# Kernel tuning notes

Hardware: AMD Instinct MI355X
Metric: run time of the kernel (lower is better)

Reference implementation:

```python
import jax, jax.numpy as jnp
import numpy as np

B, T, D, H = 32, 2048, 256, 256  # batch, length, input_size, hidden_size


def _lstm_layer(x, W_ih, W_hh, b, reverse):
    """Single-direction LSTM over time. x: [B,T,Din]; W_ih: [4H,Din]; W_hh: [4H,H]; b: [4H].
    Gate order: i, f, g, o (PyTorch convention). Returns hidden states [B,T,H]."""
    # Precompute input contribution for all timesteps in one big GEMM.
    xg = jnp.einsum('btd,gd->btg', x, W_ih) + b  # [B,T,4H]
    Hh = W_hh.shape[1]
    Bb = x.shape[0]

    def step(carry, xg_t):
        h, c = carry
        g = xg_t + h @ W_hh.T  # [B,4H]
        i, f, gc, o = jnp.split(g, 4, axis=-1)
        c = jax.nn.sigmoid(f) * c + jax.nn.sigmoid(i) * jnp.tanh(gc)
        h = jax.nn.sigmoid(o) * jnp.tanh(c)
        return (h, c), h

    init = (jnp.zeros((Bb, Hh), x.dtype), jnp.zeros((Bb, Hh), x.dtype))
    _, hs = jax.lax.scan(step, init, jnp.swapaxes(xg, 0, 1), reverse=reverse)  # [T,B,H]
    return jnp.swapaxes(hs, 0, 1)  # [B,T,H]


def setup_inputs() -> dict:
    key = jax.random.key(0)
    ks = jax.random.split(key, 13)
    s = 0.05
    G = 4 * H
    inp = {
        'x': jax.random.normal(ks[0], (B, T, D), dtype=jnp.float32),
        # layer 0 (input size D), forward and reverse directions
        'W_ih_f0': jax.random.normal(ks[1], (G, D), dtype=jnp.float32) * s,
        'W_hh_f0': jax.random.normal(ks[2], (G, H), dtype=jnp.float32) * s,
        'b_f0': jnp.zeros((G,), dtype=jnp.float32),
        'W_ih_r0': jax.random.normal(ks[3], (G, D), dtype=jnp.float32) * s,
        'W_hh_r0': jax.random.normal(ks[4], (G, H), dtype=jnp.float32) * s,
        'b_r0': jnp.zeros((G,), dtype=jnp.float32),
        # layer 1 (input size 2H because bidirectional)
        'W_ih_f1': jax.random.normal(ks[5], (G, 2 * H), dtype=jnp.float32) * s,
        'W_hh_f1': jax.random.normal(ks[6], (G, H), dtype=jnp.float32) * s,
        'b_f1': jnp.zeros((G,), dtype=jnp.float32),
        'W_ih_r1': jax.random.normal(ks[7], (G, 2 * H), dtype=jnp.float32) * s,
        'W_hh_r1': jax.random.normal(ks[8], (G, H), dtype=jnp.float32) * s,
        'b_r1': jnp.zeros((G,), dtype=jnp.float32),
    }
    return inp


def reference(x, W_ih_f0, W_hh_f0, b_f0, W_ih_r0, W_hh_r0, b_r0,
              W_ih_f1, W_hh_f1, b_f1, W_ih_r1, W_hh_r1, b_r1):
    # Layer 0: bidirectional over raw input
    h0 = jnp.concatenate([
        _lstm_layer(x, W_ih_f0, W_hh_f0, b_f0, reverse=False),
        _lstm_layer(x, W_ih_r0, W_hh_r0, b_r0, reverse=True),
    ], axis=-1)  # [B,T,2H]
    # Layer 1: bidirectional over concatenated hidden states
    h1 = jnp.concatenate([
        _lstm_layer(h0, W_ih_f1, W_hh_f1, b_f1, reverse=False),
        _lstm_layer(h0, W_ih_r1, W_hh_r1, b_r1, reverse=True),
    ], axis=-1)  # [B,T,2H]
    return h1
```

## Files before the change

### kernel.cpp

```cpp
#include <hip/hip_runtime.h>
#include <stdint.h>


#define Bn 32
#define Tn 2048
#define Hn 256

typedef short short8 __attribute__((ext_vector_type(8)));
typedef float f32x4 __attribute__((ext_vector_type(4)));
typedef unsigned int u32x4 __attribute__((ext_vector_type(4)));

__device__ inline unsigned short f2b(float f) {
  union { float f; unsigned u; } v; v.f = f;
  unsigned r = v.u + 0x7fffu + ((v.u >> 16) & 1u);
  return (unsigned short)(r >> 16);
}
__device__ inline float asf(unsigned u) {
  union { unsigned u; float f; } v; v.u = u; return v.f;
}
__device__ inline float sigx(float x) {
  return __builtin_amdgcn_rcpf(1.f + __expf(-x));
}
__device__ inline float tanhx(float x) {
  return 2.f * __builtin_amdgcn_rcpf(1.f + __expf(-2.f * x)) - 1.f;
}

template <int K, bool AF32>
__global__ __launch_bounds__(256, 2) void xg_gemm(
    const void* __restrict__ Ain,
    const float* __restrict__ Wf, const float* __restrict__ bf_,
    const float* __restrict__ Wr, const float* __restrict__ br_,
    unsigned short* __restrict__ xg) {
  constexpr int KI = K / 32;
  const int bid = blockIdx.x;
  const int scan = bid & 1;
  const int sgrp = (bid >> 1) & 7;
  const int mchunk = bid >> 4;
  const int wave = threadIdx.x >> 6;
  const int lane = threadIdx.x & 63;
  const int l15 = lane & 15, quad = lane >> 4;
  const int stripe = sgrp * 4 + wave;
  const int gi0 = stripe * 32;
  const int wp = stripe & 7;
  const int gg = stripe >> 3;

  const float* W = scan ? Wr : Wf;
  const float* bias = scan ? br_ : bf_;

  short8 bfr[KI][2];
  float bias2[2];
#pragma unroll
  for (int sub = 0; sub < 2; ++sub) {
    const int gi = gi0 + sub * 16 + l15;
    bias2[sub] = bias[gi];
#pragma unroll
    for (int ki = 0; ki < KI; ++ki) {
      const float* src = W + (size_t)gi * K + ki * 32 + quad * 8;
      short8 v;
#pragma unroll
      for (int j = 0; j < 8; ++j) v[j] = (short)f2b(src[j]);
      bfr[ki][sub] = v;
    }
  }

  const size_t scanoff = (size_t)scan << 26;
#pragma unroll 1
  for (int mt0 = 0; mt0 < 16; ++mt0) {
    const int mt = mchunk * 16 + mt0;
    const size_t row = (size_t)mt * 16 + l15;
    f32x4 acc[2];
#pragma unroll
    for (int sub = 0; sub < 2; ++sub) {
      f32x4 bi = {bias2[sub], bias2[sub], bias2[sub], bias2[sub]};
      acc[sub] = bi;
    }
#pragma unroll
    for (int ki = 0; ki < KI; ++ki) {
      short8 af;
      if constexpr (AF32) {
        const float* ap = (const float*)Ain + row * K + ki * 32 + quad * 8;
        f32x4 a0 = *(const f32x4*)ap;
        f32x4 a1 = *(const f32x4*)(ap + 4);
#pragma unroll
        for (int j = 0; j < 4; ++j) { af[j] = (short)f2b(a0[j]); af[4 + j] = (short)f2b(a1[j]); }
      } else {
        const unsigned short* ap = (const unsigned short*)Ain + row * K + ki * 32 + quad * 8;
        af = *(const short8*)ap;
      }
#pragma unroll
      for (int sub = 0; sub < 2; ++sub)
        acc[sub] = __builtin_amdgcn_mfma_f32_16x16x32_bf16(af, bfr[ki][sub], acc[sub], 0, 0, 0);
    }
#pragma unroll
    for (int sub = 0; sub < 2; ++sub) {
#pragma unroll
      for (int r = 0; r < 4; ++r) {
        const int orow = mt * 16 + quad * 4 + r;
        const int m = orow >> 11, t = orow & 2047;
        size_t idx = scanoff
          + ((((size_t)t * 2 + (m >> 4)) * 8 + wp) << 11)
          + ((size_t)((((m >> 2) & 3) << 4) + l15) << 5)
          + (sub << 4) + (gg << 2) + (m & 3);
        xg[idx] = f2b(acc[sub][r]);
      }
    }
  }
}

template <bool LAYER1>
__global__ __launch_bounds__(512, 2) void lstm_scan(
    const unsigned short* __restrict__ xg,
    const float* __restrict__ Whh_f, const float* __restrict__ Whh_r,
    unsigned short* __restrict__ h0out,
    float* __restrict__ dout) {
  __shared__ __align__(16) char smem[131072 + 2 * 8448];

  const int bid = blockIdx.x;
  const int scan = bid & 1;
  const int mh = bid >> 1;
  const int wave = threadIdx.x >> 6;
  const int lane = threadIdx.x & 63;
  const int l15 = lane & 15, quad = lane >> 4;

  const float* Whh = scan ? Whh_r : Whh_f;

  short8 wres[2][3][8];
#pragma unroll
  for (int uh = 0; uh < 2; ++uh)
#pragma unroll
    for (int g = 0; g < 3; ++g)
#pragma unroll
      for (int ki = 0; ki < 8; ++ki) {
        const int col = g * 256 + wave * 32 + uh * 16 + l15;
        const float* src = Whh + ((size_t)col << 8) + ki * 32 + quad * 8;
        f32x4 a0 = *(const f32x4*)src;
        f32x4 a1 = *(const f32x4*)(src + 4);
        short8 v;
#pragma unroll
        for (int j = 0; j < 4; ++j) { v[j] = (short)f2b(a0[j]); v[4 + j] = (short)f2b(a1[j]); }
        wres[uh][g][ki] = v;
      }
#pragma unroll
  for (int uh = 0; uh < 2; ++uh)
#pragma unroll
    for (int ki = 0; ki < 8; ++ki) {
      const int col = 768 + wave * 32 + uh * 16 + l15;
      const float* src = Whh + ((size_t)col << 8) + ki * 32 + quad * 8;
      f32x4 a0 = *(const f32x4*)src;
      f32x4 a1 = *(const f32x4*)(src + 4);
      short8 v;
#pragma unroll
      for (int j = 0; j < 4; ++j) { v[j] = (short)f2b(a0[j]); v[4 + j] = (short)f2b(a1[j]); }
      *(short8*)(smem + ((((wave << 1) + uh) << 3) + ki) * 1024 + lane * 16) = v;
    }

  const size_t scanoff = (size_t)scan << 26;
  const int tstep = scan ? -1 : 1;
  const int t0 = scan ? (Tn - 1) : 0;
  const size_t lane_off = (size_t)lane * 32;
  u32x4 xr[2][2];
  {
    const unsigned short* xb =
        xg + scanoff + ((((size_t)t0 * 2 + mh) * 8 + wave) << 11) + lane_off;
    xr[0][0] = *(const u32x4*)(xb + 0);
    xr[0][1] = *(const u32x4*)(xb + 8);
    xr[1][0] = *(const u32x4*)(xb + 16);
    xr[1][1] = *(const u32x4*)(xb + 24);
  }

  char* hbuf = smem + 131072;
  float c_st[2][4] = {{0.f, 0.f, 0.f, 0.f}, {0.f, 0.f, 0.f, 0.f}};

  __syncthreads();

#pragma unroll 1
  for (int s = 0; s < Tn; ++s) {
    const int t = scan ? (Tn - 1 - s) : s;
    const int tn = (s < Tn - 1) ? (t + tstep) : t;
    const unsigned short* xbn =
        xg + scanoff + ((((size_t)tn * 2 + mh) * 8 + wave) << 11) + lane_off;
    const int p_r = (s - 1) & 1, p_w = s & 1;

#pragma unroll
    for (int uh = 0; uh < 2; ++uh) {
      f32x4 acc[4];
#pragma unroll
      for (int g = 0; g < 4; ++g) {
        unsigned lo = xr[uh][g >> 1][2 * (g & 1)];
        unsigned hi = xr[uh][g >> 1][2 * (g & 1) + 1];
        acc[g][0] = asf(lo << 16); acc[g][1] = asf(lo & 0xffff0000u);
        acc[g][2] = asf(hi << 16); acc[g][3] = asf(hi & 0xffff0000u);
      }
      if (uh == 1) {
        xr[0][0] = *(const u32x4*)(xbn + 0);
        xr[0][1] = *(const u32x4*)(xbn + 8);
      }

      if (s > 0) {
        const char* hr = hbuf + p_r * 8448 + l15 * 528 + quad * 16;
        const char* wl0 = smem + (((wave << 1) + uh) << 13) + lane * 16;
#pragma unroll
        for (int ki = 0; ki < 8; ++ki) {
          short8 a = *(const short8*)(hr + (ki << 6));
          short8 wl = *(const short8*)(wl0 + (ki << 10));
          acc[0] = __builtin_amdgcn_mfma_f32_16x16x32_bf16(a, wres[uh][0][ki], acc[0], 0, 0, 0);
          acc[1] = __builtin_amdgcn_mfma_f32_16x16x32_bf16(a, wres[uh][1][ki], acc[1], 0, 0, 0);
          acc[2] = __builtin_amdgcn_mfma_f32_16x16x32_bf16(a, wres[uh][2][ki], acc[2], 0, 0, 0);
          acc[3] = __builtin_amdgcn_mfma_f32_16x16x32_bf16(a, wl,              acc[3], 0, 0, 0);
        }
      }

      const int ubase = wave * 32 + uh * 16 + l15;
#pragma unroll
      for (int r = 0; r < 4; ++r) {
        float ig = sigx(acc[0][r]), fg = sigx(acc[1][r]);
        float gc = tanhx(acc[2][r]), og = sigx(acc[3][r]);
        float cv = fg * c_st[uh][r] + ig * gc;
        c_st[uh][r] = cv;
        float hv = og * tanhx(cv);
        unsigned short h16 = f2b(hv);
        int pk = __shfl_xor((int)h16, 1);
        const int row = quad * 4 + r;
        if (!(lane & 1)) {
          unsigned pv = (unsigned)h16 | ((unsigned)pk << 16);
          *(unsigned*)(hbuf + p_w * 8448 + row * 528 + ubase * 2) = pv;
        }
        const int b = mh * 16 + row;
        if constexpr (!LAYER1) {
          h0out[(((size_t)b * Tn + t) << 9) + scan * Hn + ubase] = h16;
        } else {
          dout[(((size_t)b * Tn + t) << 9) + scan * Hn + ubase] = hv;
        }
      }

      if (uh == 1) {
        xr[1][0] = *(const u32x4*)(xbn + 16);
        xr[1][1] = *(const u32x4*)(xbn + 24);
      }
    }

    __syncthreads();
  }
}

extern "C" void kernel_launch(void* const* d_in, const int* in_sizes, int n_in,
                              void* d_out, int out_size, void* d_ws, size_t ws_size,
                              hipStream_t stream) {
  (void)in_sizes; (void)n_in; (void)out_size; (void)ws_size;
  const float* x      = (const float*)d_in[0];
  const float* Wih_f0 = (const float*)d_in[1];
  const float* Whh_f0 = (const float*)d_in[2];
  const float* b_f0   = (const float*)d_in[3];
  const float* Wih_r0 = (const float*)d_in[4];
  const float* Whh_r0 = (const float*)d_in[5];
  const float* b_r0   = (const float*)d_in[6];
  const float* Wih_f1 = (const float*)d_in[7];
  const float* Whh_f1 = (const float*)d_in[8];
  const float* b_f1   = (const float*)d_in[9];
  const float* Wih_r1 = (const float*)d_in[10];
  const float* Whh_r1 = (const float*)d_in[11];
  const float* b_r1   = (const float*)d_in[12];

  char* ws = (char*)d_ws;
  unsigned short* xgbuf = (unsigned short*)ws;
  size_t off = (size_t)2 * Tn * Bn * 1024 * sizeof(unsigned short);
  unsigned short* h0out = (unsigned short*)(ws + off);

  dim3 blkA(256), blkB(512);
  xg_gemm<256, true><<<dim3(4096), blkA, 0, stream>>>(
      (const void*)x, Wih_f0, b_f0, Wih_r0, b_r0, xgbuf);
  lstm_scan<false><<<dim3(4), blkB, 0, stream>>>(
      xgbuf, Whh_f0, Whh_r0, h0out, (float*)nullptr);
  xg_gemm<512, false><<<dim3(4096), blkA, 0, stream>>>(
      (const void*)h0out, Wih_f1, b_f1, Wih_r1, b_r1, xgbuf);
  lstm_scan<true><<<dim3(4), blkB, 0, stream>>>(
      xgbuf, Whh_f1, Whh_r1, (unsigned short*)nullptr, (float*)d_out);
}
```

Before: 14.15 ms.

## Fold log2(e) scaling into weights and swizzle h buffer into MFMA fragment layout

Pre-scales the input and recurrent weights and biases by log2(e) (2·log2(e) for the cell gate) so the gate nonlinearities can call native exp2 directly, saving a multiply per transcendental on the serial per-step path. The cell state is kept scaled by 2·log2(e), which shifts the tanh into a sigmoid-based form. The hidden-state shared buffer moves from a padded row-major layout to a fragment-ordered layout, so each lane reads its MFMA A operand with one contiguous 16-byte load. The pre-scaling is applied before bf16 rounding, which slightly changes the numerics.

```diff
diff --git a/kernel.cpp b/kernel.cpp
--- a/kernel.cpp
+++ b/kernel.cpp
@@ -6,9 +6,15 @@
 #define Tn 2048
 #define Hn 256
 
+#define L2E 1.4426950408889634f
+#define L2E2 2.8853900817779268f
+#define L2E4 5.7707801635558535f
+
 typedef short short8 __attribute__((ext_vector_type(8)));
 typedef float f32x4 __attribute__((ext_vector_type(4)));
 typedef unsigned int u32x4 __attribute__((ext_vector_type(4)));
+
+extern "C" __device__ float __ocml_native_exp2_f32(float);
 
 __device__ inline unsigned short f2b(float f) {
   union { float f; unsigned u; } v; v.f = f;
@@ -18,11 +24,8 @@
 __device__ inline float asf(unsigned u) {
   union { unsigned u; float f; } v; v.u = u; return v.f;
 }
-__device__ inline float sigx(float x) {
-  return __builtin_amdgcn_rcpf(1.f + __expf(-x));
-}
-__device__ inline float tanhx(float x) {
-  return 2.f * __builtin_amdgcn_rcpf(1.f + __expf(-2.f * x)) - 1.f;
+__device__ inline float sig2(float x) {
+  return __builtin_amdgcn_rcpf(1.f + __ocml_native_exp2_f32(-x));
 }
 
 template <int K, bool AF32>
@@ -46,19 +49,20 @@
 
   const float* W = scan ? Wr : Wf;
   const float* bias = scan ? br_ : bf_;
+  const float gscale = (gg == 2) ? L2E2 : L2E;
 
   short8 bfr[KI][2];
   float bias2[2];
 #pragma unroll
   for (int sub = 0; sub < 2; ++sub) {
     const int gi = gi0 + sub * 16 + l15;
-    bias2[sub] = bias[gi];
+    bias2[sub] = bias[gi] * gscale;
 #pragma unroll
     for (int ki = 0; ki < KI; ++ki) {
       const float* src = W + (size_t)gi * K + ki * 32 + quad * 8;
       short8 v;
 #pragma unroll
-      for (int j = 0; j < 8; ++j) v[j] = (short)f2b(src[j]);
+      for (int j = 0; j < 8; ++j) v[j] = (short)f2b(src[j] * gscale);
       bfr[ki][sub] = v;
     }
   }
@@ -113,7 +117,7 @@
     const float* __restrict__ Whh_f, const float* __restrict__ Whh_r,
     unsigned short* __restrict__ h0out,
     float* __restrict__ dout) {
-  __shared__ __align__(16) char smem[131072 + 2 * 8448];
+  __shared__ __align__(16) char smem[131072 + 2 * 8192];
 
   const int bid = blockIdx.x;
   const int scan = bid & 1;
@@ -128,7 +132,8 @@
 #pragma unroll
   for (int uh = 0; uh < 2; ++uh)
 #pragma unroll
-    for (int g = 0; g < 3; ++g)
+    for (int g = 0; g < 3; ++g) {
+      const float ws = (g == 2) ? L2E2 : L2E;
 #pragma unroll
       for (int ki = 0; ki < 8; ++ki) {
         const int col = g * 256 + wave * 32 + uh * 16 + l15;
@@ -137,9 +142,10 @@
         f32x4 a1 = *(const f32x4*)(src + 4);
         short8 v;
 #pragma unroll
-        for (int j = 0; j < 4; ++j) { v[j] = (short)f2b(a0[j]); v[4 + j] = (short)f2b(a1[j]); }
+        for (int j = 0; j < 4; ++j) { v[j] = (short)f2b(a0[j] * ws); v[4 + j] = (short)f2b(a1[j] * ws); }
         wres[uh][g][ki] = v;
       }
+    }
 #pragma unroll
   for (int uh = 0; uh < 2; ++uh)
 #pragma unroll
@@ -150,7 +156,7 @@
       f32x4 a1 = *(const f32x4*)(src + 4);
       short8 v;
 #pragma unroll
-      for (int j = 0; j < 4; ++j) { v[j] = (short)f2b(a0[j]); v[4 + j] = (short)f2b(a1[j]); }
+      for (int j = 0; j < 4; ++j) { v[j] = (short)f2b(a0[j] * L2E); v[4 + j] = (short)f2b(a1[j] * L2E); }
       *(short8*)(smem + ((((wave << 1) + uh) << 3) + ki) * 1024 + lane * 16) = v;
     }
 
@@ -197,11 +203,11 @@
       }
 
       if (s > 0) {
-        const char* hr = hbuf + p_r * 8448 + l15 * 528 + quad * 16;
+        const char* hr = hbuf + p_r * 8192 + lane * 16;
         const char* wl0 = smem + (((wave << 1) + uh) << 13) + lane * 16;
 #pragma unroll
         for (int ki = 0; ki < 8; ++ki) {
-          short8 a = *(const short8*)(hr + (ki << 6));
+          short8 a = *(const short8*)(hr + (ki << 10));
           short8 wl = *(const short8*)(wl0 + (ki << 10));
           acc[0] = __builtin_amdgcn_mfma_f32_16x16x32_bf16(a, wres[uh][0][ki], acc[0], 0, 0, 0);
           acc[1] = __builtin_amdgcn_mfma_f32_16x16x32_bf16(a, wres[uh][1][ki], acc[1], 0, 0, 0);
@@ -211,19 +217,23 @@
       }
 
       const int ubase = wave * 32 + uh * 16 + l15;
+      char* hwb = hbuf + p_w * 8192 + wave * 1024 +
+                  ((uh * 2 + (l15 >> 3)) << 8) + (l15 & 7) * 2;
 #pragma unroll
       for (int r = 0; r < 4; ++r) {
-        float ig = sigx(acc[0][r]), fg = sigx(acc[1][r]);
-        float gc = tanhx(acc[2][r]), og = sigx(acc[3][r]);
-        float cv = fg * c_st[uh][r] + ig * gc;
+        float ig = sig2(acc[0][r]);
+        float fg = sig2(acc[1][r]);
+        float gt = __builtin_fmaf(sig2(acc[2][r]), L2E4, -L2E2);
+        float og = sig2(acc[3][r]);
+        float cv = __builtin_fmaf(fg, c_st[uh][r], ig * gt);
         c_st[uh][r] = cv;
-        float hv = og * tanhx(cv);
+        float hv = og * __builtin_fmaf(sig2(cv), 2.f, -1.f);
         unsigned short h16 = f2b(hv);
         int pk = __shfl_xor((int)h16, 1);
         const int row = quad * 4 + r;
         if (!(lane & 1)) {
           unsigned pv = (unsigned)h16 | ((unsigned)pk << 16);
-          *(unsigned*)(hbuf + p_w * 8448 + row * 528 + ubase * 2) = pv;
+          *(unsigned*)(hwb + row * 16) = pv;
         }
         const int b = mh * 16 + row;
         if constexpr (!LAYER1) {
```

Measured after the change: 14.87 ms. +5.1%, slower.
